# Performance work log

Measured on AMD Instinct MI355X. Metric: run time of the kernel, lower is better.

The kernel has to match this reference:

```python
import jax, jax.numpy as jnp
import numpy as np
from jax import lax

L, B, T_IMG, T_TXT = 12, 2, 256, 64
E, H, G = 1024, 16, 2730
V = 16416  # image_vocab_count + 1
C = E // H
EPS = 1e-6  # flax LayerNorm default


def _ln(x, scale, bias):
    mu = jnp.mean(x, -1, keepdims=True)
    var = jnp.var(x, -1, keepdims=True)
    y = (x - mu) * lax.rsqrt(var + EPS)
    if scale is not None:
        y = y * scale
    if bias is not None:
        y = y + bias
    return y


def _attend(k, v, q, mask, o_w):
    # k,v: [B,K,H,C]  q: [B,Q,H,C]  mask: [B,K]
    bias = jnp.where(mask, 0.0, -jnp.inf)[:, None, None, :]
    w = jnp.einsum('bqhc,bkhc->bhqk', q, k) + bias
    w = jax.nn.softmax(w, axis=-1)
    out = jnp.einsum('bhqk,bkhc->bqhc', w, v)
    return out.reshape(out.shape[0], out.shape[1], E) @ o_w


def setup_inputs():
    key = jax.random.key(0)
    ks = jax.random.split(key, 16)
    s = 0.02
    n = lambda k, shape: jax.random.normal(k, shape, jnp.float32) * s
    return dict(
        encoder_state=n(ks[0], (B, T_TXT, E)),
        keys_state=jnp.zeros((L, B, T_IMG, H, C), jnp.float32),
        values_state=jnp.zeros((L, B, T_IMG, H, C), jnp.float32),
        attention_mask=jnp.ones((B, T_TXT), jnp.bool_),
        prev_token=5000,
        token_index=100,
        embed_tok=n(ks[1], (V, E)),
        embed_pos=n(ks[2], (T_IMG, E)),
        ln_emb_s=jnp.ones((E,), jnp.float32),
        ln_emb_b=jnp.zeros((E,), jnp.float32),
        final_ln_b=jnp.zeros((E,), jnp.float32),
        lm_head_w=n(ks[3], (E, V)),
        pre_sa_ln_b=jnp.zeros((L, E), jnp.float32),
        sa_q_w=n(ks[4], (L, E, E)), sa_k_w=n(ks[5], (L, E, E)),
        sa_v_w=n(ks[6], (L, E, E)), sa_o_w=n(ks[7], (L, E, E)),
        sa_ln_s=jnp.ones((L, E), jnp.float32), sa_ln_b=jnp.zeros((L, E), jnp.float32),
        pre_ca_ln_b=jnp.zeros((L, E), jnp.float32),
        ca_q_w=n(ks[8], (L, E, E)), ca_k_w=n(ks[9], (L, E, E)),
        ca_v_w=n(ks[10], (L, E, E)), ca_o_w=n(ks[11], (L, E, E)),
        ca_ln_s=jnp.ones((L, E), jnp.float32), ca_ln_b=jnp.zeros((L, E), jnp.float32),
        glu_ln0_b=jnp.zeros((L, E), jnp.float32),
        glu_fc0_w=n(ks[12], (L, E, G)), glu_fc1_w=n(ks[13], (L, E, G)),
        glu_ln1_b=jnp.zeros((L, G), jnp.float32),
        glu_fc2_w=n(ks[14], (L, G, E)),
    )


def _decode_step(encoder_state, keys_state, values_state, attention_mask,
                 prev_token, token_index, embed_tok, embed_pos,
                 ln_emb_s, ln_emb_b, final_ln_b, lm_head_w, layer_params):
    ones = jnp.ones((B, 1), jnp.int32)
    ds = embed_tok[prev_token * ones] + embed_pos[token_index * ones]  # [B,1,E]
    ds = _ln(ds, ln_emb_s, ln_emb_b)
    self_mask = jnp.broadcast_to(jnp.arange(T_IMG) < token_index + 1, (B, T_IMG))
    scale = C ** 0.5

    def step(ds, xs):
        ks_l, vs_l, p = xs  # per-layer KV cache [B,T_IMG,H,C] and params
        (pre_sa_b, qw, kw, vw, ow, sa_s, sa_b,
         pre_ca_b, cqw, ckw, cvw, cow, ca_s, ca_b,
         g0b, f0, f1, g1b, f2) = p
        # --- self attention with KV-cache append ---
        residual = ds
        x = _ln(ds, None, pre_sa_b)
        ks_l = lax.dynamic_update_slice(ks_l, (x @ kw).reshape(B, 1, H, C), (0, token_index, 0, 0))
        vs_l = lax.dynamic_update_slice(vs_l, (x @ vw).reshape(B, 1, H, C), (0, token_index, 0, 0))
        q = (x @ qw).reshape(B, 1, H, C) / scale
        x = _attend(ks_l, vs_l, q, self_mask, ow)
        ds = residual + _ln(x, sa_s, sa_b)
        # --- cross attention over encoder state ---
        residual = ds
        x = _ln(ds, None, pre_ca_b)
        ek = (encoder_state @ ckw).reshape(B, T_TXT, H, C)
        ev = (encoder_state @ cvw).reshape(B, T_TXT, H, C)
        q = (x @ cqw).reshape(B, 1, H, C) / scale
        x = _attend(ek, ev, q, attention_mask, cow)
        ds = residual + _ln(x, ca_s, ca_b)
        # --- GLU FFN ---
        residual = ds
        z = _ln(ds, None, g0b)
        w = jax.nn.gelu(z @ f0, approximate=False)
        z = _ln(w * (z @ f1), None, g1b)
        ds = residual + z @ f2
        return ds, (ks_l, vs_l)

    ds, (keys_state, values_state) = lax.scan(step, ds, (keys_state, values_state, layer_params))
    ds = _ln(ds, None, final_ln_b)
    logits = ds @ lm_head_w  # [B,1,V]
    return logits, keys_state, values_state


def reference(encoder_state, keys_state, values_state, attention_mask, prev_token,
              token_index, embed_tok, embed_pos, ln_emb_s, ln_emb_b, final_ln_b,
              lm_head_w, pre_sa_ln_b, sa_q_w, sa_k_w, sa_v_w, sa_o_w, sa_ln_s,
              sa_ln_b, pre_ca_ln_b, ca_q_w, ca_k_w, ca_v_w, ca_o_w, ca_ln_s,
              ca_ln_b, glu_ln0_b, glu_fc0_w, glu_fc1_w, glu_ln1_b, glu_fc2_w):
    layer_params = (pre_sa_ln_b, sa_q_w, sa_k_w, sa_v_w, sa_o_w, sa_ln_s, sa_ln_b,
                    pre_ca_ln_b, ca_q_w, ca_k_w, ca_v_w, ca_o_w, ca_ln_s, ca_ln_b,
                    glu_ln0_b, glu_fc0_w, glu_fc1_w, glu_ln1_b, glu_fc2_w)
    return _decode_step(encoder_state, keys_state, values_state, attention_mask,
                        prev_token, token_index, embed_tok, embed_pos,
                        ln_emb_s, ln_emb_b, final_ln_b, lm_head_w, layer_params)
```

## Files before the change

### kernel.cpp

```cpp
#include <hip/hip_runtime.h>
#include <math.h>

#define LAYERS 12
#define EE 1024
#define GG 2730
#define VV 16416
#define EPS 1e-6f

#define OFF_DS 0
#define NSLOT 37
#define OFF_ACC (OFF_DS + NSLOT*2048)
#define ACC_STRIDE 28672
#define AQ 0
#define AK 2048
#define AV 4096
#define AY 6144
#define AQC 8192
#define ASC 10240
#define AOUT 12288
#define AY2 14336
#define AA 16384
#define AB2 21844
#define ACC_TOTAL (LAYERS*ACC_STRIDE)
#define ZERO_FLOATS (NSLOT*2048 + ACC_TOTAL)

#define KVL 524288
#define KVB 262144

struct MegaP {
  const float* enc; const float* keys_in; const float* values_in;
  const int* maski; const int* pt; const int* ti;
  const float* tok; const float* pos; const float* ln_s; const float* ln_b;
  const float* final_b; const float* lm_w;
  const float* pre_sa_b; const float* saq; const float* sak; const float* sav;
  const float* sao; const float* sas; const float* sab;
  const float* pre_ca_b; const float* caq; const float* ckw; const float* cvw;
  const float* cao; const float* cas; const float* cab;
  const float* g0b; const float* f0; const float* f1; const float* g1b; const float* f2;
  float* logits; float* keys_out; float* values_out; float* ws;
};

__device__ __forceinline__ void red4(float* sm, float& a, float& b, float& c, float& d){
  #pragma unroll
  for(int o=32;o;o>>=1){ a+=__shfl_down(a,o); b+=__shfl_down(b,o); c+=__shfl_down(c,o); d+=__shfl_down(d,o); }
  int w=threadIdx.x>>6, l=threadIdx.x&63;
  __syncthreads();
  if(l==0){ sm[w]=a; sm[4+w]=b; sm[8+w]=c; sm[12+w]=d; }
  __syncthreads();
  a=sm[0]+sm[1]+sm[2]+sm[3]; b=sm[4]+sm[5]+sm[6]+sm[7];
  c=sm[8]+sm[9]+sm[10]+sm[11]; d=sm[12]+sm[13]+sm[14]+sm[15];
}

__device__ __forceinline__ void ln_stats_g(const float* v, int K, float* sm,
    float& mu0, float& rs0, float& mu1, float& rs1){
  float s0=0,q0=0,s1=0,q1=0;
  for(int i=threadIdx.x;i<K;i+=256){ float a=v[i], b=v[K+i]; s0+=a;q0+=a*a;s1+=b;q1+=b*b; }
  red4(sm,s0,q0,s1,q1);
  mu0=s0/K; mu1=s1/K;
  rs0=rsqrtf(fmaxf(q0/K-mu0*mu0,0.f)+EPS);
  rs1=rsqrtf(fmaxf(q1/K-mu1*mu1,0.f)+EPS);
}

__device__ __forceinline__ void ln_stats_l(float (*Ds)[1024], float* sm,
    float& mu0, float& rs0, float& mu1, float& rs1){
  float s0=0,q0=0,s1=0,q1=0;
  for(int i=threadIdx.x;i<EE;i+=256){ float a=Ds[0][i], b=Ds[1][i]; s0+=a;q0+=a*a;s1+=b;q1+=b*b; }
  red4(sm,s0,q0,s1,q1);
  mu0=s0/EE; mu1=s1/EE;
  rs0=rsqrtf(fmaxf(q0/EE-mu0*mu0,0.f)+EPS);
  rs1=rsqrtf(fmaxf(q1/EE-mu1*mu1,0.f)+EPS);
}

__device__ __forceinline__ void build_ds3(const float* dsi, const float* accL,
    const float* sasl, const float* sabl, const float* casl, const float* cabl,
    float (*Ds)[1024], float* sm){
  float mu0,rs0,mu1,rs1;
  ln_stats_g(accL+AY, EE, sm, mu0,rs0,mu1,rs1);
  for(int i=threadIdx.x;i<EE;i+=256){ float sc=sasl[i], bi=sabl[i];
    Ds[0][i]=dsi[i]    + (accL[AY+i]-mu0)*rs0*sc + bi;
    Ds[1][i]=dsi[EE+i] + (accL[AY+EE+i]-mu1)*rs1*sc + bi; }
  ln_stats_g(accL+AY2, EE, sm, mu0,rs0,mu1,rs1);
  for(int i=threadIdx.x;i<EE;i+=256){ float sc=casl[i], bi=cabl[i];
    Ds[0][i] += (accL[AY2+i]-mu0)*rs0*sc + bi;
    Ds[1][i] += (accL[AY2+EE+i]-mu1)*rs1*sc + bi; }
}

__global__ __launch_bounds__(256)
void k_prelude(MegaP p){
  __shared__ float ev[EE];
  __shared__ float sm[16];
  const int t=threadIdx.x;
  int ptv = p.pt[0], tiv = p.ti[0];
  float s0=0,q0=0,d1=0,d2=0;
  for(int i=t;i<EE;i+=256){ float v=p.tok[(size_t)ptv*EE+i]+p.pos[(size_t)tiv*EE+i]; ev[i]=v; s0+=v; q0+=v*v; }
  red4(sm,s0,q0,d1,d2);
  float mu=s0/EE, rs=rsqrtf(fmaxf(q0/EE-mu*mu,0.f)+EPS);
  float* ds0 = p.ws + OFF_DS;
  __syncthreads();
  for(int i=t;i<EE;i+=256){ float y=(ev[i]-mu)*rs*p.ln_s[i]+p.ln_b[i]; ds0[i]=y; ds0[EE+i]=y; }
}

__global__ __launch_bounds__(256)
void k_qkv(MegaP p, int l){
  __shared__ float Xs[2][1024];
  __shared__ float sm[16];
  const int t=threadIdx.x, bx=blockIdx.x, by=blockIdx.y;
  if (bx >= 12){
    int cb = (bx-12)*64 + by;
    #pragma unroll
    for(int j=0;j<4;j++){
      int idx4 = cb*1024 + j*256 + t;
      int kv = idx4 >> 17;
      int r4 = idx4 & 131071;
      size_t off = (size_t)l*KVL + (size_t)r4*4;
      float4 v = *(const float4*)((kv? p.values_in : p.keys_in) + off);
      *(float4*)((kv? p.values_out : p.keys_out) + off) = v;
    }
    return;
  }
  const float* dsi = p.ws + OFF_DS + (size_t)(3*l)*2048;
  float* accL = p.ws + OFF_ACC + (size_t)l*ACC_STRIDE;
  const size_t lE2=(size_t)l*EE*EE, lE=(size_t)l*EE;
  int c = bx*256 + t;
  int sel = c>>10, cc = c&1023;
  const float* W = (sel==0? p.saq : sel==1? p.sak : p.sav) + lE2;
  float* O = accL + (sel==0? AQ : sel==1? AK : AV);
  int k0 = by*16;
  const float* wp = W + (size_t)k0*EE + cc;
  float wr[16];
  #pragma unroll
  for(int k=0;k<16;k++) wr[k] = wp[(size_t)k*EE];
  float mu0,rs0,mu1,rs1;
  ln_stats_g(dsi, EE, sm, mu0,rs0,mu1,rs1);
  for(int i=t;i<EE;i+=256){ float bi=p.pre_sa_b[lE+i];
    Xs[0][i]=(dsi[i]-mu0)*rs0+bi; Xs[1][i]=(dsi[EE+i]-mu1)*rs1+bi; }
  __syncthreads();
  float a0=0,a1=0;
  #pragma unroll
  for(int k=0;k<16;k++){ a0+=Xs[0][k0+k]*wr[k]; a1+=Xs[1][k0+k]*wr[k]; }
  atomicAdd(&O[cc],a0); atomicAdd(&O[EE+cc],a1);
}

__global__ __launch_bounds__(256)
void k_selfo(MegaP p, int l){
  __shared__ float Ds[2][1024];
  __shared__ float att[2][256];
  __shared__ float sm[16];
  const int t=threadIdx.x, bkid=blockIdx.x, tiv=p.ti[0];
  float* accL = p.ws + OFF_ACC + (size_t)l*ACC_STRIDE;
  const size_t lE2=(size_t)l*EE*EE;
  int cg=bkid&3, h=(bkid>>2)&15, sub=(bkid>>6)&3, hoff=h*64;
  if (t < 128){ int bb2=t>>6, c2=t&63; Ds[bb2][c2] = accL[AQ + bb2*EE + hoff + c2]*0.125f; }
  __syncthreads();
  for(int bb2=0;bb2<2;bb2++)
    for(int tt=t; tt<=tiv; tt+=256){
      const float* kr = (tt<tiv) ? (p.keys_in + (size_t)l*KVL + (size_t)bb2*KVB + (size_t)tt*EE + hoff)
                                 : (accL + AK + bb2*EE + hoff);
      float d=0;
      #pragma unroll
      for(int c2=0;c2<64;c2++) d += Ds[bb2][c2]*kr[c2];
      att[bb2][tt] = d;
    }
  __syncthreads();
  int wv=t>>6, l2=t&63;
  if (wv<2){
    float m=-3.4e38f;
    for(int tt=l2; tt<=tiv; tt+=64) m=fmaxf(m, att[wv][tt]);
    #pragma unroll
    for(int o=32;o;o>>=1) m=fmaxf(m,__shfl_xor(m,o));
    float s=0;
    for(int tt=l2; tt<=tiv; tt+=64){ float e=__expf(att[wv][tt]-m); att[wv][tt]=e; s+=e; }
    #pragma unroll
    for(int o=32;o;o>>=1) s+=__shfl_xor(s,o);
    if(l2==0) sm[8+wv]=1.f/s;
  }
  __syncthreads();
  {
    int bb2=t>>7, j=(t>>3)&15, part=t&7, colh=sub*16+j;
    float v=0;
    for(int tt=part; tt<=tiv; tt+=8){
      float vv = (tt<tiv)? p.values_in[(size_t)l*KVL + (size_t)bb2*KVB + (size_t)tt*EE + hoff + colh]
                         : accL[AV + bb2*EE + hoff + colh];
      v += att[bb2][tt]*vv;
    }
    v += __shfl_down(v,4,8); v += __shfl_down(v,2,8); v += __shfl_down(v,1,8);
    if(part==0) Ds[bb2][512+j] = v*sm[8+bb2];
  }
  __syncthreads();
  {
    int c = cg*256+t, kb = hoff + sub*16;
    const float* wp = p.sao + lE2 + (size_t)kb*EE + c;
    float a0=0,a1=0;
    #pragma unroll
    for(int j2=0;j2<16;j2++){ float w=wp[(size_t)j2*EE]; a0+=Ds[0][512+j2]*w; a1+=Ds[1][512+j2]*w; }
    atomicAdd(&accL[AY+c],a0); atomicAdd(&accL[AY+EE+c],a1);
  }
  if (cg==0 && sub==0){
    int bb2=t>>7, kv=(t>>6)&1, c2=t&63;
    float val = accL[(kv?AV:AK) + bb2*EE + hoff + c2];
    float* dst = (kv? p.values_out : p.keys_out)
               + (size_t)l*KVL + (size_t)bb2*KVB + (size_t)tiv*EE + hoff + c2;
    *dst = val;
  }
}

__global__ __launch_bounds__(256)
void k_ds2caq(MegaP p, int l){
  __shared__ float Xs[2][1024];
  __shared__ float Ds[2][1024];
  __shared__ float sm[16];
  const int t=threadIdx.x;
  const float* dsi = p.ws + OFF_DS + (size_t)(3*l)*2048;
  float* accL = p.ws + OFF_ACC + (size_t)l*ACC_STRIDE;
  const size_t lE2=(size_t)l*EE*EE, lE=(size_t)l*EE;
  int c = blockIdx.x*256 + t;
  int k0 = blockIdx.y*16;
  const float* wp = p.caq + lE2 + (size_t)k0*EE + c;
  float wr[16];
  #pragma unroll
  for(int k=0;k<16;k++) wr[k] = wp[(size_t)k*EE];
  float mu0,rs0,mu1,rs1;
  ln_stats_g(accL+AY, EE, sm, mu0,rs0,mu1,rs1);
  for(int i=t;i<EE;i+=256){ float sc=p.sas[lE+i], bi=p.sab[lE+i];
    Ds[0][i]=dsi[i]    + (accL[AY+i]-mu0)*rs0*sc + bi;
    Ds[1][i]=dsi[EE+i] + (accL[AY+EE+i]-mu1)*rs1*sc + bi; }
  ln_stats_l(Ds, sm, mu0,rs0,mu1,rs1);
  for(int i=t;i<EE;i+=256){ float bi=p.pre_ca_b[lE+i];
    Xs[0][i]=(Ds[0][i]-mu0)*rs0+bi; Xs[1][i]=(Ds[1][i]-mu1)*rs1+bi; }
  __syncthreads();
  float a0=0,a1=0;
  #pragma unroll
  for(int k=0;k<16;k++){ a0+=Xs[0][k0+k]*wr[k]; a1+=Xs[1][k0+k]*wr[k]; }
  float* O = accL + AQC;
  atomicAdd(&O[c],a0); atomicAdd(&O[EE+c],a1);
}

__global__ __launch_bounds__(256)
void k_uscore(MegaP p, int l){
  __shared__ float qs[64];
  __shared__ float us[256];
  const int t=threadIdx.x, bh=blockIdx.x, ec=blockIdx.y;
  const int b=bh>>4, h=bh&15, hoff=h*64;
  float* accL = p.ws + OFF_ACC + (size_t)l*ACC_STRIDE;
  const size_t lE2=(size_t)l*EE*EE;
  const int e = ec*256 + t;
  const float4* cp = (const float4*)(p.ckw + lE2 + (size_t)e*EE + hoff);
  float4 wr[16];
  #pragma unroll
  for(int j=0;j<16;j++) wr[j] = cp[j];
  if (t < 64) qs[t] = accL[AQC + b*EE + hoff + t]*0.125f;
  __syncthreads();
  float u=0;
  #pragma unroll
  for(int j=0;j<16;j++){
    u += wr[j].x*qs[4*j] + wr[j].y*qs[4*j+1] + wr[j].z*qs[4*j+2] + wr[j].w*qs[4*j+3];
  }
  us[t]=u;
  __syncthreads();
  int t2=t&63, q4=t>>6;
  const float4* ep = (const float4*)(p.enc + (size_t)(b*64+t2)*EE + ec*256 + q4*64);
  float pa=0;
  #pragma unroll
  for(int j=0;j<16;j++){
    float4 e4=ep[j];
    pa += e4.x*us[q4*64+4*j] + e4.y*us[q4*64+4*j+1] + e4.z*us[q4*64+4*j+2] + e4.w*us[q4*64+4*j+3];
  }
  atomicAdd(&accL[ASC + (b*16+h)*64 + t2], pa);
}

__global__ __launch_bounds__(256)
void k_ov(MegaP p, int l){
  __shared__ float att[64];
  __shared__ float ctxp[2][128];
  __shared__ float ctxs[128];
  __shared__ float smr[2];
  const int t=threadIdx.x, bh=blockIdx.x, es=blockIdx.y;
  const int b=bh>>4, h=bh&15, hoff=h*64, e0=es*128;
  float* accL = p.ws + OFF_ACC + (size_t)l*ACC_STRIDE;
  const size_t lE2=(size_t)l*EE*EE;
  const int c=t&63, part=t>>6;
  const float* vp = p.cvw + lE2 + (size_t)(e0+part*32)*EE + hoff + c;
  float wr[32];
  #pragma unroll
  for(int j=0;j<32;j++) wr[j] = vp[(size_t)j*EE];
  if (t<64){
    float sc = accL[ASC + (b*16+h)*64 + t];
    int mi=b*64+t;
    bool valid = (p.maski[mi]!=0) || (((const unsigned char*)p.maski)[mi]!=0);
    sc = valid? sc : -3.4e38f;
    float m=sc;
    #pragma unroll
    for(int o=32;o;o>>=1) m=fmaxf(m,__shfl_xor(m,o));
    float e_ = valid? __expf(sc-m) : 0.f;
    float s=e_;
    #pragma unroll
    for(int o=32;o;o>>=1) s+=__shfl_xor(s,o);
    att[t]=e_;
    if(t==0) smr[0]=1.f/s;
  }
  __syncthreads();
  {
    int e2=t>>1, half=t&1;
    const float* ep = p.enc + (size_t)(b*64+half*32)*EE + e0+e2;
    float ca=0;
    #pragma unroll 8
    for(int tt=0;tt<32;tt++) ca += att[half*32+tt]*ep[(size_t)tt*EE];
    ctxp[half][e2]=ca;
  }
  __syncthreads();
  if (t<128) ctxs[t] = (ctxp[0][t]+ctxp[1][t])*smr[0];
  __syncthreads();
  float a=0;
  #pragma unroll
  for(int j=0;j<32;j++) a += ctxs[part*32+j]*wr[j];
  atomicAdd(&accL[AOUT + b*EE + hoff + c], a);
}

__global__ __launch_bounds__(256)
void k_y2(MegaP p, int l){
  __shared__ float Xs[2][1024];
  const int t=threadIdx.x;
  float* accL = p.ws + OFF_ACC + (size_t)l*ACC_STRIDE;
  const size_t lE2=(size_t)l*EE*EE;
  int c = blockIdx.x*256 + t;
  int k0 = blockIdx.y*16;
  const float* wp = p.cao + lE2 + (size_t)k0*EE + c;
  float wr[16];
  #pragma unroll
  for(int k=0;k<16;k++) wr[k] = wp[(size_t)k*EE];
  for(int i=t;i<EE;i+=256){ Xs[0][i]=accL[AOUT+i]; Xs[1][i]=accL[AOUT+EE+i]; }
  __syncthreads();
  float a0=0,a1=0;
  #pragma unroll
  for(int k=0;k<16;k++){ a0+=Xs[0][k0+k]*wr[k]; a1+=Xs[1][k0+k]*wr[k]; }
  atomicAdd(&accL[AY2+c],a0); atomicAdd(&accL[AY2+EE+c],a1);
}

__global__ __launch_bounds__(256)
void k_glu01(MegaP p, int l){
  __shared__ float Xs[2][1024];
  __shared__ float Ds[2][1024];
  __shared__ float sm[16];
  const int t=threadIdx.x;
  const float* dsi = p.ws + OFF_DS + (size_t)(3*l)*2048;
  float* accL = p.ws + OFF_ACC + (size_t)l*ACC_STRIDE;
  const size_t lEG=(size_t)l*EE*GG, lE=(size_t)l*EE;
  int c2 = blockIdx.x*256 + t;
  int k0 = blockIdx.y*16;
  int sel=0, col=0;
  const float* W = nullptr;
  float2 wr[16];
  if (c2 < 2730){
    sel = (c2>=1365); int cc2 = sel? c2-1365 : c2; col = cc2*2;
    W = (sel? p.f1 : p.f0) + lEG;
    const float2* wp = (const float2*)(W + (size_t)k0*GG + col);
    #pragma unroll
    for(int k=0;k<16;k++) wr[k] = wp[(size_t)k*1365];
  }
  build_ds3(dsi, accL, p.sas+lE, p.sab+lE, p.cas+lE, p.cab+lE, Ds, sm);
  float mu0,rs0,mu1,rs1;
  ln_stats_l(Ds, sm, mu0,rs0,mu1,rs1);
  for(int i=t;i<EE;i+=256){ float bi=p.g0b[lE+i];
    Xs[0][i]=(Ds[0][i]-mu0)*rs0+bi; Xs[1][i]=(Ds[1][i]-mu1)*rs1+bi; }
  __syncthreads();
  if (c2 < 2730){
    float* O = accL + (sel? AB2 : AA);
    float a0=0,a1=0,b0=0,b1=0;
    #pragma unroll
    for(int k=0;k<16;k++){
      float x0=Xs[0][k0+k], x1=Xs[1][k0+k];
      a0+=x0*wr[k].x; a1+=x0*wr[k].y; b0+=x1*wr[k].x; b1+=x1*wr[k].y;
    }
    atomicAdd(&O[col+0],a0); atomicAdd(&O[col+1],a1);
    atomicAdd(&O[GG+col+0],b0); atomicAdd(&O[GG+col+1],b1);
  }
}

__global__ __launch_bounds__(256)
void k_glu2(MegaP p, int l){
  __shared__ float Xs[2][2736];
  __shared__ float Ds[2][1024];
  __shared__ float sm[16];
  const int t=threadIdx.x;
  const float* dsi = p.ws + OFF_DS + (size_t)(3*l)*2048;
  float* ds4 = p.ws + OFF_DS + (size_t)(3*l+3)*2048;
  float* accL = p.ws + OFF_ACC + (size_t)l*ACC_STRIDE;
  const size_t lGE=(size_t)l*GG*EE, lE=(size_t)l*EE, lG=(size_t)l*GG;
  const int ks = blockIdx.y;
  int c = blockIdx.x*256 + t;
  int k0 = ks*32, k1 = k0+32; if (k1>GG) k1=GG;
  const float* wp = p.f2 + lGE + (size_t)k0*EE + c;
  float wr[32];
  #pragma unroll
  for(int k=0;k<32;k++) wr[k] = (k0+k<GG) ? wp[(size_t)k*EE] : 0.f;
  if (ks==0) build_ds3(dsi, accL, p.sas+lE, p.sab+lE, p.cas+lE, p.cab+lE, Ds, sm);
  float s0=0,q0=0,s1=0,q1=0;
  for(int i=t;i<GG;i+=256){
    float a0v=accL[AA+i], a1v=accL[AA+GG+i];
    float b0v=accL[AB2+i], b1v=accL[AB2+GG+i];
    float g0v=0.5f*a0v*(1.f+erff(a0v*0.70710678118654752f));
    float g1v=0.5f*a1v*(1.f+erff(a1v*0.70710678118654752f));
    float t0=g0v*b0v, t1=g1v*b1v;
    Xs[0][i]=t0; Xs[1][i]=t1;
    s0+=t0;q0+=t0*t0;s1+=t1;q1+=t1*t1;
  }
  red4(sm,s0,q0,s1,q1);
  float mu0=s0/GG, mu1=s1/GG;
  float rs0=rsqrtf(fmaxf(q0/GG-mu0*mu0,0.f)+EPS), rs1=rsqrtf(fmaxf(q1/GG-mu1*mu1,0.f)+EPS);
  for(int i=t;i<GG;i+=256){ float bi=p.g1b[lG+i];
    Xs[0][i]=(Xs[0][i]-mu0)*rs0+bi; Xs[1][i]=(Xs[1][i]-mu1)*rs1+bi; }
  __syncthreads();
  float a0=0,b0=0;
  if (ks==0){ a0=Ds[0][c]; b0=Ds[1][c]; }
  #pragma unroll
  for(int k=0;k<32;k++){
    if (k0+k<GG){ a0+=Xs[0][k0+k]*wr[k]; b0+=Xs[1][k0+k]*wr[k]; }
  }
  atomicAdd(&ds4[c],a0); atomicAdd(&ds4[EE+c],b0);
}

__global__ __launch_bounds__(256)
void k_lm(MegaP p){
  __shared__ float Xs[2][1024];
  __shared__ float sm[16];
  const int t=threadIdx.x;
  const float* dsf = p.ws + OFF_DS + (size_t)36*2048;
  float mu0,rs0,mu1,rs1;
  ln_stats_g(dsf, EE, sm, mu0,rs0,mu1,rs1);
  for(int i=t;i<EE;i+=256){ float bi=p.final_b[i];
    Xs[0][i]=(dsf[i]-mu0)*rs0+bi; Xs[1][i]=(dsf[EE+i]-mu1)*rs1+bi; }
  __syncthreads();
  int c4 = blockIdx.x*256 + t;
  if (c4 < 4104){
    int col = c4*4;
    int k0 = blockIdx.y*32;
    const float4* wp = (const float4*)(p.lm_w + (size_t)k0*VV + col);
    float a0=0,a1=0,a2=0,a3=0,b0=0,b1=0,b2=0,b3=0;
    #pragma unroll 8
    for(int k=0;k<32;k++){
      float4 w=*wp; wp+=4104;
      float x0=Xs[0][k0+k], x1=Xs[1][k0+k];
      a0+=x0*w.x; a1+=x0*w.y; a2+=x0*w.z; a3+=x0*w.w;
      b0+=x1*w.x; b1+=x1*w.y; b2+=x1*w.z; b3+=x1*w.w;
    }
    atomicAdd(&p.logits[col+0],a0); atomicAdd(&p.logits[col+1],a1);
    atomicAdd(&p.logits[col+2],a2); atomicAdd(&p.logits[col+3],a3);
    atomicAdd(&p.logits[VV+col+0],b0); atomicAdd(&p.logits[VV+col+1],b1);
    atomicAdd(&p.logits[VV+col+2],b2); atomicAdd(&p.logits[VV+col+3],b3);
  }
}

extern "C" void kernel_launch(void* const* d_in, const int* in_sizes, int n_in,
                              void* d_out, int out_size, void* d_ws, size_t ws_size,
                              hipStream_t stream){
  (void)in_sizes; (void)n_in; (void)out_size; (void)ws_size;
  float* out = (float*)d_out;
  float* ws = (float*)d_ws;

  MegaP P;
  P.enc        = (const float*)d_in[0];
  P.keys_in    = (const float*)d_in[1];
  P.values_in  = (const float*)d_in[2];
  P.maski      = (const int*)d_in[3];
  P.pt         = (const int*)d_in[4];
  P.ti         = (const int*)d_in[5];
  P.tok        = (const float*)d_in[6];
  P.pos        = (const float*)d_in[7];
  P.ln_s       = (const float*)d_in[8];
  P.ln_b       = (const float*)d_in[9];
  P.final_b    = (const float*)d_in[10];
  P.lm_w       = (const float*)d_in[11];
  P.pre_sa_b   = (const float*)d_in[12];
  P.saq        = (const float*)d_in[13];
  P.sak        = (const float*)d_in[14];
  P.sav        = (const float*)d_in[15];
  P.sao        = (const float*)d_in[16];
  P.sas        = (const float*)d_in[17];
  P.sab        = (const float*)d_in[18];
  P.pre_ca_b   = (const float*)d_in[19];
  P.caq        = (const float*)d_in[20];
  P.ckw        = (const float*)d_in[21];
  P.cvw        = (const float*)d_in[22];
  P.cao        = (const float*)d_in[23];
  P.cas        = (const float*)d_in[24];
  P.cab        = (const float*)d_in[25];
  P.g0b        = (const float*)d_in[26];
  P.f0         = (const float*)d_in[27];
  P.f1         = (const float*)d_in[28];
  P.g1b        = (const float*)d_in[29];
  P.f2         = (const float*)d_in[30];
  P.logits     = out;
  P.keys_out   = out + (size_t)2*VV;
  P.values_out = P.keys_out + (size_t)LAYERS*KVL;
  P.ws         = ws;

  hipMemsetAsync(ws + OFF_DS, 0, (size_t)ZERO_FLOATS*sizeof(float), stream);
  hipMemsetAsync(P.logits, 0, (size_t)2*VV*sizeof(float), stream);

  k_prelude<<<1,256,0,stream>>>(P);
  for (int l=0;l<LAYERS;l++){
    k_qkv   <<<dim3(16,64),256,0,stream>>>(P,l);
    k_selfo <<<256,        256,0,stream>>>(P,l);
    k_ds2caq<<<dim3(4,64), 256,0,stream>>>(P,l);
    k_uscore<<<dim3(32,4), 256,0,stream>>>(P,l);
    k_ov    <<<dim3(32,8), 256,0,stream>>>(P,l);
    k_y2    <<<dim3(4,64), 256,0,stream>>>(P,l);
    k_glu01 <<<dim3(11,64),256,0,stream>>>(P,l);
    k_glu2  <<<dim3(4,86), 256,0,stream>>>(P,l);
  }
  k_lm<<<dim3(17,32),256,0,stream>>>(P);
}
```

Baseline: 1.065 ms.

## Fuse cross-attention chain into one per-head kernel with 1024 threads

Replaces the four cross-attention kernels (LN plus Q projection, key-score, softmax plus value/output, output projection) with one kernel. Each of the 32 blocks handles one (batch, head) pair and keeps all intermediates in shared memory. This removes three launches and the global atomic round trips between stages per layer. In exchange only 32 blocks run, each streaming its own head slice of four weight matrices through serialized phases, with Q and K weights read once per batch. That risks low GPU occupancy and a latency-bound weight stream.

```diff
diff --git a/kernel.cpp b/kernel.cpp
--- a/kernel.cpp
+++ b/kernel.cpp
@@ -51,6 +51,18 @@
   c=sm[8]+sm[9]+sm[10]+sm[11]; d=sm[12]+sm[13]+sm[14]+sm[15];
 }
 
+__device__ __forceinline__ void red2_1024(float* sm, float& a, float& b){
+  #pragma unroll
+  for(int o=32;o;o>>=1){ a+=__shfl_down(a,o); b+=__shfl_down(b,o); }
+  int w=threadIdx.x>>6, l=threadIdx.x&63;
+  __syncthreads();
+  if(l==0){ sm[w]=a; sm[16+w]=b; }
+  __syncthreads();
+  a=0; b=0;
+  #pragma unroll
+  for(int j=0;j<16;j++){ a+=sm[j]; b+=sm[16+j]; }
+}
+
 __device__ __forceinline__ void ln_stats_g(const float* v, int K, float* sm,
     float& mu0, float& rs0, float& mu1, float& rs1){
   float s0=0,q0=0,s1=0,q1=0;
@@ -204,136 +216,124 @@
   }
 }
 
-__global__ __launch_bounds__(256)
-void k_ds2caq(MegaP p, int l){
-  __shared__ float Xs[2][1024];
-  __shared__ float Ds[2][1024];
-  __shared__ float sm[16];
-  const int t=threadIdx.x;
+__global__ __launch_bounds__(1024)
+void k_cross(MegaP p, int l){
+  __shared__ float Xs[1024];
+  __shared__ float P[1024];
+  __shared__ float us[1024];
+  __shared__ float Cx[1024];
+  __shared__ float att[64];
+  __shared__ float outh[64];
+  __shared__ float sm[32];
+  const int t=threadIdx.x, bi=blockIdx.x;
+  const int b=bi>>4, h=bi&15, hoff=h*64;
+  float* accL = p.ws + OFF_ACC + (size_t)l*ACC_STRIDE;
   const float* dsi = p.ws + OFF_DS + (size_t)(3*l)*2048;
-  float* accL = p.ws + OFF_ACC + (size_t)l*ACC_STRIDE;
   const size_t lE2=(size_t)l*EE*EE, lE=(size_t)l*EE;
-  int c = blockIdx.x*256 + t;
-  int k0 = blockIdx.y*16;
-  const float* wp = p.caq + lE2 + (size_t)k0*EE + c;
-  float wr[16];
-  #pragma unroll
-  for(int k=0;k<16;k++) wr[k] = wp[(size_t)k*EE];
-  float mu0,rs0,mu1,rs1;
-  ln_stats_g(accL+AY, EE, sm, mu0,rs0,mu1,rs1);
-  for(int i=t;i<EE;i+=256){ float sc=p.sas[lE+i], bi=p.sab[lE+i];
-    Ds[0][i]=dsi[i]    + (accL[AY+i]-mu0)*rs0*sc + bi;
-    Ds[1][i]=dsi[EE+i] + (accL[AY+EE+i]-mu1)*rs1*sc + bi; }
-  ln_stats_l(Ds, sm, mu0,rs0,mu1,rs1);
-  for(int i=t;i<EE;i+=256){ float bi=p.pre_ca_b[lE+i];
-    Xs[0][i]=(Ds[0][i]-mu0)*rs0+bi; Xs[1][i]=(Ds[1][i]-mu1)*rs1+bi; }
-  __syncthreads();
-  float a0=0,a1=0;
-  #pragma unroll
-  for(int k=0;k<16;k++){ a0+=Xs[0][k0+k]*wr[k]; a1+=Xs[1][k0+k]*wr[k]; }
-  float* O = accL + AQC;
-  atomicAdd(&O[c],a0); atomicAdd(&O[EE+c],a1);
-}
-
-__global__ __launch_bounds__(256)
-void k_uscore(MegaP p, int l){
-  __shared__ float qs[64];
-  __shared__ float us[256];
-  const int t=threadIdx.x, bh=blockIdx.x, ec=blockIdx.y;
-  const int b=bh>>4, h=bh&15, hoff=h*64;
-  float* accL = p.ws + OFF_ACC + (size_t)l*ACC_STRIDE;
-  const size_t lE2=(size_t)l*EE*EE;
-  const int e = ec*256 + t;
-  const float4* cp = (const float4*)(p.ckw + lE2 + (size_t)e*EE + hoff);
-  float4 wr[16];
-  #pragma unroll
-  for(int j=0;j<16;j++) wr[j] = cp[j];
-  if (t < 64) qs[t] = accL[AQC + b*EE + hoff + t]*0.125f;
-  __syncthreads();
-  float u=0;
-  #pragma unroll
-  for(int j=0;j<16;j++){
-    u += wr[j].x*qs[4*j] + wr[j].y*qs[4*j+1] + wr[j].z*qs[4*j+2] + wr[j].w*qs[4*j+3];
-  }
-  us[t]=u;
-  __syncthreads();
-  int t2=t&63, q4=t>>6;
-  const float4* ep = (const float4*)(p.enc + (size_t)(b*64+t2)*EE + ec*256 + q4*64);
-  float pa=0;
-  #pragma unroll
-  for(int j=0;j<16;j++){
-    float4 e4=ep[j];
-    pa += e4.x*us[q4*64+4*j] + e4.y*us[q4*64+4*j+1] + e4.z*us[q4*64+4*j+2] + e4.w*us[q4*64+4*j+3];
-  }
-  atomicAdd(&accL[ASC + (b*16+h)*64 + t2], pa);
-}
-
-__global__ __launch_bounds__(256)
-void k_ov(MegaP p, int l){
-  __shared__ float att[64];
-  __shared__ float ctxp[2][128];
-  __shared__ float ctxs[128];
-  __shared__ float smr[2];
-  const int t=threadIdx.x, bh=blockIdx.x, es=blockIdx.y;
-  const int b=bh>>4, h=bh&15, hoff=h*64, e0=es*128;
-  float* accL = p.ws + OFF_ACC + (size_t)l*ACC_STRIDE;
-  const size_t lE2=(size_t)l*EE*EE;
-  const int c=t&63, part=t>>6;
-  const float* vp = p.cvw + lE2 + (size_t)(e0+part*32)*EE + hoff + c;
-  float wr[32];
-  #pragma unroll
-  for(int j=0;j<32;j++) wr[j] = vp[(size_t)j*EE];
+
+  float yv = accL[AY + b*EE + t];
+  float s0=yv, q0=yv*yv;
+  red2_1024(sm, s0, q0);
+  float mu=s0/EE, rs=rsqrtf(fmaxf(q0/EE-mu*mu,0.f)+EPS);
+  float ds2v = dsi[b*EE+t] + (yv-mu)*rs*p.sas[lE+t] + p.sab[lE+t];
+  s0=ds2v; q0=ds2v*ds2v;
+  __syncthreads();
+  red2_1024(sm, s0, q0);
+  mu=s0/EE; rs=rsqrtf(fmaxf(q0/EE-mu*mu,0.f)+EPS);
+  Xs[t] = (ds2v-mu)*rs + p.pre_ca_b[lE+t];
+  __syncthreads();
+
+  {
+    int c=t&63, kp=t>>6;
+    const float* cqp = p.caq + lE2 + (size_t)(kp*64)*EE + hoff + c;
+    float pq=0;
+    #pragma unroll 8
+    for(int j=0;j<64;j++) pq += Xs[kp*64+j]*cqp[(size_t)j*EE];
+    P[t]=pq;
+  }
+  __syncthreads();
   if (t<64){
-    float sc = accL[ASC + (b*16+h)*64 + t];
+    float q=0;
+    #pragma unroll
+    for(int kp=0;kp<16;kp++) q += P[kp*64+t];
+    us[t] = q*0.125f;
+  }
+  __syncthreads();
+  if (t<64) att[t]=us[t];
+  __syncthreads();
+
+  {
+    const float4* ckp = (const float4*)(p.ckw + lE2 + (size_t)t*EE + hoff);
+    float u=0;
+    #pragma unroll
+    for(int j=0;j<16;j++){
+      float4 w=ckp[j];
+      u += w.x*att[4*j] + w.y*att[4*j+1] + w.z*att[4*j+2] + w.w*att[4*j+3];
+    }
+    us[t]=u;
+  }
+  __syncthreads();
+
+  {
+    int tt=t>>4, ep=t&15;
+    const float* erow = p.enc + (size_t)(b*64+tt)*EE + ep*64;
+    float ps=0;
+    #pragma unroll 8
+    for(int j=0;j<64;j++) ps += us[ep*64+j]*erow[j];
+    P[t]=ps;
+  }
+  __syncthreads();
+  if (t<64){
+    float sc=0;
+    #pragma unroll
+    for(int ep=0;ep<16;ep++) sc += P[t*16+ep];
     int mi=b*64+t;
     bool valid = (p.maski[mi]!=0) || (((const unsigned char*)p.maski)[mi]!=0);
     sc = valid? sc : -3.4e38f;
     float m=sc;
     #pragma unroll
     for(int o=32;o;o>>=1) m=fmaxf(m,__shfl_xor(m,o));
-    float e_ = valid? __expf(sc-m) : 0.f;
+    float e_=valid? __expf(sc-m):0.f;
     float s=e_;
     #pragma unroll
     for(int o=32;o;o>>=1) s+=__shfl_xor(s,o);
-    att[t]=e_;
-    if(t==0) smr[0]=1.f/s;
-  }
-  __syncthreads();
-  {
-    int e2=t>>1, half=t&1;
-    const float* ep = p.enc + (size_t)(b*64+half*32)*EE + e0+e2;
-    float ca=0;
+    att[t]=e_/s;
+  }
+  __syncthreads();
+
+  {
+    const float* encB = p.enc + (size_t)(b*64)*EE + t;
+    float cv=0;
     #pragma unroll 8
-    for(int tt=0;tt<32;tt++) ca += att[half*32+tt]*ep[(size_t)tt*EE];
-    ctxp[half][e2]=ca;
-  }
-  __syncthreads();
-  if (t<128) ctxs[t] = (ctxp[0][t]+ctxp[1][t])*smr[0];
-  __syncthreads();
-  float a=0;
-  #pragma unroll
-  for(int j=0;j<32;j++) a += ctxs[part*32+j]*wr[j];
-  atomicAdd(&accL[AOUT + b*EE + hoff + c], a);
-}
-
-__global__ __launch_bounds__(256)
-void k_y2(MegaP p, int l){
-  __shared__ float Xs[2][1024];
-  const int t=threadIdx.x;
-  float* accL = p.ws + OFF_ACC + (size_t)l*ACC_STRIDE;
-  const size_t lE2=(size_t)l*EE*EE;
-  int c = blockIdx.x*256 + t;
-  int k0 = blockIdx.y*16;
-  const float* wp = p.cao + lE2 + (size_t)k0*EE + c;
-  float wr[16];
-  #pragma unroll
-  for(int k=0;k<16;k++) wr[k] = wp[(size_t)k*EE];
-  for(int i=t;i<EE;i+=256){ Xs[0][i]=accL[AOUT+i]; Xs[1][i]=accL[AOUT+EE+i]; }
-  __syncthreads();
-  float a0=0,a1=0;
-  #pragma unroll
-  for(int k=0;k<16;k++){ a0+=Xs[0][k0+k]*wr[k]; a1+=Xs[1][k0+k]*wr[k]; }
-  atomicAdd(&accL[AY2+c],a0); atomicAdd(&accL[AY2+EE+c],a1);
+    for(int tt=0;tt<64;tt++) cv += att[tt]*encB[(size_t)tt*EE];
+    Cx[t]=cv;
+  }
+  __syncthreads();
+
+  {
+    int c=t&63, ep=t>>6;
+    const float* cvp = p.cvw + lE2 + (size_t)(ep*64)*EE + hoff + c;
+    float po=0;
+    #pragma unroll 8
+    for(int j=0;j<64;j++) po += Cx[ep*64+j]*cvp[(size_t)j*EE];
+    P[t]=po;
+  }
+  __syncthreads();
+  if (t<64){
+    float o=0;
+    #pragma unroll
+    for(int ep=0;ep<16;ep++) o += P[ep*64+t];
+    outh[t]=o;
+  }
+  __syncthreads();
+
+  {
+    const float* cop = p.cao + lE2 + (size_t)hoff*EE + t;
+    float y=0;
+    #pragma unroll 8
+    for(int c2=0;c2<64;c2++) y += outh[c2]*cop[(size_t)c2*EE];
+    atomicAdd(&accL[AY2 + b*EE + t], y);
+  }
 }
 
 __global__ __launch_bounds__(256)
@@ -501,10 +501,7 @@
   for (int l=0;l<LAYERS;l++){
     k_qkv   <<<dim3(16,64),256,0,stream>>>(P,l);
     k_selfo <<<256,        256,0,stream>>>(P,l);
-    k_ds2caq<<<dim3(4,64), 256,0,stream>>>(P,l);
-    k_uscore<<<dim3(32,4), 256,0,stream>>>(P,l);
-    k_ov    <<<dim3(32,8), 256,0,stream>>>(P,l);
-    k_y2    <<<dim3(4,64), 256,0,stream>>>(P,l);
+    k_cross <<<32,        1024,0,stream>>>(P,l);
     k_glu01 <<<dim3(11,64),256,0,stream>>>(P,l);
     k_glu2  <<<dim3(4,86), 256,0,stream>>>(P,l);
   }
```

After: 1.271 ms. 1.19x slower.

## Fuse cross-attn value and output projections; vectorize weight loads in GEMV kernels

Applied to the files above, without the earlier changes.

Merges the cross-attention context/value kernel and the output-projection kernel into one. Each block now projects its partial per-head output straight through its 64-row slice of the output weights and atomically accumulates into the residual, which removes one launch and the AOUT round trip. The QKV, cross-attention query and GLU fc2 GEMVs switch to float4/float2 weight loads with several columns per thread, and their grids and K-splits are re-shaped to match; the KV cache copy moves into one column of QKV blocks. The cost is that the fused kernel re-reads each head's output-weight slice from every (batch, e-slice) block and issues many more atomics.

```diff
diff --git a/kernel.cpp b/kernel.cpp
--- a/kernel.cpp
+++ b/kernel.cpp
@@ -17,7 +17,6 @@
 #define AY 6144
 #define AQC 8192
 #define ASC 10240
-#define AOUT 12288
 #define AY2 14336
 #define AA 16384
 #define AB2 21844
@@ -105,11 +104,11 @@
   __shared__ float Xs[2][1024];
   __shared__ float sm[16];
   const int t=threadIdx.x, bx=blockIdx.x, by=blockIdx.y;
-  if (bx >= 12){
-    int cb = (bx-12)*64 + by;
-    #pragma unroll
-    for(int j=0;j<4;j++){
-      int idx4 = cb*1024 + j*256 + t;
+  if (bx == 3){
+    int cb = by;
+    #pragma unroll
+    for(int j=0;j<8;j++){
+      int idx4 = cb*2048 + j*256 + t;
       int kv = idx4 >> 17;
       int r4 = idx4 & 131071;
       size_t off = (size_t)l*KVL + (size_t)r4*4;
@@ -121,24 +120,29 @@
   const float* dsi = p.ws + OFF_DS + (size_t)(3*l)*2048;
   float* accL = p.ws + OFF_ACC + (size_t)l*ACC_STRIDE;
   const size_t lE2=(size_t)l*EE*EE, lE=(size_t)l*EE;
-  int c = bx*256 + t;
-  int sel = c>>10, cc = c&1023;
+  int c4 = bx*256 + t;
+  int col = c4*4, sel = col>>10, cc = col&1023;
   const float* W = (sel==0? p.saq : sel==1? p.sak : p.sav) + lE2;
   float* O = accL + (sel==0? AQ : sel==1? AK : AV);
-  int k0 = by*16;
-  const float* wp = W + (size_t)k0*EE + cc;
-  float wr[16];
-  #pragma unroll
-  for(int k=0;k<16;k++) wr[k] = wp[(size_t)k*EE];
+  int k0 = by*8;
+  const float4* wp = (const float4*)(W + (size_t)k0*EE + cc);
+  float4 wr[8];
+  #pragma unroll
+  for(int k=0;k<8;k++) wr[k] = wp[(size_t)k*256];
   float mu0,rs0,mu1,rs1;
   ln_stats_g(dsi, EE, sm, mu0,rs0,mu1,rs1);
   for(int i=t;i<EE;i+=256){ float bi=p.pre_sa_b[lE+i];
     Xs[0][i]=(dsi[i]-mu0)*rs0+bi; Xs[1][i]=(dsi[EE+i]-mu1)*rs1+bi; }
   __syncthreads();
-  float a0=0,a1=0;
-  #pragma unroll
-  for(int k=0;k<16;k++){ a0+=Xs[0][k0+k]*wr[k]; a1+=Xs[1][k0+k]*wr[k]; }
-  atomicAdd(&O[cc],a0); atomicAdd(&O[EE+cc],a1);
+  float a0=0,a1=0,a2=0,a3=0,b0=0,b1=0,b2=0,b3=0;
+  #pragma unroll
+  for(int k=0;k<8;k++){
+    float x0=Xs[0][k0+k], x1=Xs[1][k0+k];
+    a0+=x0*wr[k].x; a1+=x0*wr[k].y; a2+=x0*wr[k].z; a3+=x0*wr[k].w;
+    b0+=x1*wr[k].x; b1+=x1*wr[k].y; b2+=x1*wr[k].z; b3+=x1*wr[k].w;
+  }
+  atomicAdd(&O[cc+0],a0); atomicAdd(&O[cc+1],a1); atomicAdd(&O[cc+2],a2); atomicAdd(&O[cc+3],a3);
+  atomicAdd(&O[EE+cc+0],b0); atomicAdd(&O[EE+cc+1],b1); atomicAdd(&O[EE+cc+2],b2); atomicAdd(&O[EE+cc+3],b3);
 }
 
 __global__ __launch_bounds__(256)
@@ -213,12 +217,12 @@
   const float* dsi = p.ws + OFF_DS + (size_t)(3*l)*2048;
   float* accL = p.ws + OFF_ACC + (size_t)l*ACC_STRIDE;
   const size_t lE2=(size_t)l*EE*EE, lE=(size_t)l*EE;
-  int c = blockIdx.x*256 + t;
-  int k0 = blockIdx.y*16;
-  const float* wp = p.caq + lE2 + (size_t)k0*EE + c;
-  float wr[16];
-  #pragma unroll
-  for(int k=0;k<16;k++) wr[k] = wp[(size_t)k*EE];
+  int col = t*4;
+  int k0 = blockIdx.x*4;
+  const float4* wp = (const float4*)(p.caq + lE2 + (size_t)k0*EE + col);
+  float4 wr[4];
+  #pragma unroll
+  for(int k=0;k<4;k++) wr[k] = wp[(size_t)k*256];
   float mu0,rs0,mu1,rs1;
   ln_stats_g(accL+AY, EE, sm, mu0,rs0,mu1,rs1);
   for(int i=t;i<EE;i+=256){ float sc=p.sas[lE+i], bi=p.sab[lE+i];
@@ -228,11 +232,16 @@
   for(int i=t;i<EE;i+=256){ float bi=p.pre_ca_b[lE+i];
     Xs[0][i]=(Ds[0][i]-mu0)*rs0+bi; Xs[1][i]=(Ds[1][i]-mu1)*rs1+bi; }
   __syncthreads();
-  float a0=0,a1=0;
-  #pragma unroll
-  for(int k=0;k<16;k++){ a0+=Xs[0][k0+k]*wr[k]; a1+=Xs[1][k0+k]*wr[k]; }
+  float a0=0,a1=0,a2=0,a3=0,b0=0,b1=0,b2=0,b3=0;
+  #pragma unroll
+  for(int k=0;k<4;k++){
+    float x0=Xs[0][k0+k], x1=Xs[1][k0+k];
+    a0+=x0*wr[k].x; a1+=x0*wr[k].y; a2+=x0*wr[k].z; a3+=x0*wr[k].w;
+    b0+=x1*wr[k].x; b1+=x1*wr[k].y; b2+=x1*wr[k].z; b3+=x1*wr[k].w;
+  }
   float* O = accL + AQC;
-  atomicAdd(&O[c],a0); atomicAdd(&O[EE+c],a1);
+  atomicAdd(&O[col+0],a0); atomicAdd(&O[col+1],a1); atomicAdd(&O[col+2],a2); atomicAdd(&O[col+3],a3);
+  atomicAdd(&O[EE+col+0],b0); atomicAdd(&O[EE+col+1],b1); atomicAdd(&O[EE+col+2],b2); atomicAdd(&O[EE+col+3],b3);
 }
 
 __global__ __launch_bounds__(256)
@@ -269,11 +278,12 @@
 }
 
 __global__ __launch_bounds__(256)
-void k_ov(MegaP p, int l){
+void k_ovy2(MegaP p, int l){
   __shared__ float att[64];
   __shared__ float ctxp[2][128];
   __shared__ float ctxs[128];
-  __shared__ float smr[2];
+  __shared__ float P[256];
+  __shared__ float outh[64];
   const int t=threadIdx.x, bh=blockIdx.x, es=blockIdx.y;
   const int b=bh>>4, h=bh&15, hoff=h*64, e0=es*128;
   float* accL = p.ws + OFF_ACC + (size_t)l*ACC_STRIDE;
@@ -295,8 +305,7 @@
     float s=e_;
     #pragma unroll
     for(int o=32;o;o>>=1) s+=__shfl_xor(s,o);
-    att[t]=e_;
-    if(t==0) smr[0]=1.f/s;
+    att[t]=e_/s;
   }
   __syncthreads();
   {
@@ -308,32 +317,26 @@
     ctxp[half][e2]=ca;
   }
   __syncthreads();
-  if (t<128) ctxs[t] = (ctxp[0][t]+ctxp[1][t])*smr[0];
-  __syncthreads();
-  float a=0;
-  #pragma unroll
-  for(int j=0;j<32;j++) a += ctxs[part*32+j]*wr[j];
-  atomicAdd(&accL[AOUT + b*EE + hoff + c], a);
-}
-
-__global__ __launch_bounds__(256)
-void k_y2(MegaP p, int l){
-  __shared__ float Xs[2][1024];
-  const int t=threadIdx.x;
-  float* accL = p.ws + OFF_ACC + (size_t)l*ACC_STRIDE;
-  const size_t lE2=(size_t)l*EE*EE;
-  int c = blockIdx.x*256 + t;
-  int k0 = blockIdx.y*16;
-  const float* wp = p.cao + lE2 + (size_t)k0*EE + c;
-  float wr[16];
-  #pragma unroll
-  for(int k=0;k<16;k++) wr[k] = wp[(size_t)k*EE];
-  for(int i=t;i<EE;i+=256){ Xs[0][i]=accL[AOUT+i]; Xs[1][i]=accL[AOUT+EE+i]; }
-  __syncthreads();
-  float a0=0,a1=0;
-  #pragma unroll
-  for(int k=0;k<16;k++){ a0+=Xs[0][k0+k]*wr[k]; a1+=Xs[1][k0+k]*wr[k]; }
-  atomicAdd(&accL[AY2+c],a0); atomicAdd(&accL[AY2+EE+c],a1);
+  if (t<128) ctxs[t] = ctxp[0][t]+ctxp[1][t];
+  __syncthreads();
+  {
+    float po=0;
+    #pragma unroll
+    for(int j=0;j<32;j++) po += ctxs[part*32+j]*wr[j];
+    P[t]=po;
+  }
+  __syncthreads();
+  if (t<64) outh[t] = P[t]+P[64+t]+P[128+t]+P[192+t];
+  __syncthreads();
+  {
+    const float* cop = p.cao + lE2 + (size_t)hoff*EE;
+    for(int n=t;n<EE;n+=256){
+      float y=0;
+      #pragma unroll 8
+      for(int c2=0;c2<64;c2++) y += outh[c2]*cop[(size_t)c2*EE + n];
+      atomicAdd(&accL[AY2 + b*EE + n], y);
+    }
+  }
 }
 
 __global__ __launch_bounds__(256)
@@ -387,12 +390,16 @@
   float* accL = p.ws + OFF_ACC + (size_t)l*ACC_STRIDE;
   const size_t lGE=(size_t)l*GG*EE, lE=(size_t)l*EE, lG=(size_t)l*GG;
   const int ks = blockIdx.y;
-  int c = blockIdx.x*256 + t;
-  int k0 = ks*32, k1 = k0+32; if (k1>GG) k1=GG;
-  const float* wp = p.f2 + lGE + (size_t)k0*EE + c;
-  float wr[32];
-  #pragma unroll
-  for(int k=0;k<32;k++) wr[k] = (k0+k<GG) ? wp[(size_t)k*EE] : 0.f;
+  int c2 = blockIdx.x*256 + t;
+  int col = c2*2;
+  int k0 = ks*16;
+  const float2* wp = (const float2*)(p.f2 + lGE + (size_t)k0*EE + col);
+  float2 wr[16];
+  #pragma unroll
+  for(int k=0;k<16;k++){
+    if (k0+k < GG) wr[k] = wp[(size_t)k*512];
+    else { wr[k].x=0.f; wr[k].y=0.f; }
+  }
   if (ks==0) build_ds3(dsi, accL, p.sas+lE, p.sab+lE, p.cas+lE, p.cab+lE, Ds, sm);
   float s0=0,q0=0,s1=0,q1=0;
   for(int i=t;i<GG;i+=256){
@@ -410,13 +417,17 @@
   for(int i=t;i<GG;i+=256){ float bi=p.g1b[lG+i];
     Xs[0][i]=(Xs[0][i]-mu0)*rs0+bi; Xs[1][i]=(Xs[1][i]-mu1)*rs1+bi; }
   __syncthreads();
-  float a0=0,b0=0;
-  if (ks==0){ a0=Ds[0][c]; b0=Ds[1][c]; }
-  #pragma unroll
-  for(int k=0;k<32;k++){
-    if (k0+k<GG){ a0+=Xs[0][k0+k]*wr[k]; b0+=Xs[1][k0+k]*wr[k]; }
-  }
-  atomicAdd(&ds4[c],a0); atomicAdd(&ds4[EE+c],b0);
+  float a0=0,a1=0,b0=0,b1=0;
+  if (ks==0){ a0=Ds[0][col]; a1=Ds[0][col+1]; b0=Ds[1][col]; b1=Ds[1][col+1]; }
+  #pragma unroll
+  for(int k=0;k<16;k++){
+    if (k0+k < GG){
+      float x0=Xs[0][k0+k], x1=Xs[1][k0+k];
+      a0+=x0*wr[k].x; a1+=x0*wr[k].y; b0+=x1*wr[k].x; b1+=x1*wr[k].y;
+    }
+  }
+  atomicAdd(&ds4[col+0],a0); atomicAdd(&ds4[col+1],a1);
+  atomicAdd(&ds4[EE+col+0],b0); atomicAdd(&ds4[EE+col+1],b1);
 }
 
 __global__ __launch_bounds__(256)
@@ -499,14 +510,13 @@
 
   k_prelude<<<1,256,0,stream>>>(P);
   for (int l=0;l<LAYERS;l++){
-    k_qkv   <<<dim3(16,64),256,0,stream>>>(P,l);
+    k_qkv   <<<dim3(4,128),256,0,stream>>>(P,l);
     k_selfo <<<256,        256,0,stream>>>(P,l);
-    k_ds2caq<<<dim3(4,64), 256,0,stream>>>(P,l);
+    k_ds2caq<<<256,        256,0,stream>>>(P,l);
     k_uscore<<<dim3(32,4), 256,0,stream>>>(P,l);
-    k_ov    <<<dim3(32,8), 256,0,stream>>>(P,l);
-    k_y2    <<<dim3(4,64), 256,0,stream>>>(P,l);
+    k_ovy2  <<<dim3(32,8), 256,0,stream>>>(P,l);
     k_glu01 <<<dim3(11,64),256,0,stream>>>(P,l);
-    k_glu2  <<<dim3(4,86), 256,0,stream>>>(P,l);
+    k_glu2  <<<dim3(2,171),256,0,stream>>>(P,l);
   }
   k_lm<<<dim3(17,32),256,0,stream>>>(P);
 }
```

After: 1.910 ms. 1.79x slower.

## Fuse cross-attention query projection into per-head score kernel

Applied to the files above, without the earlier changes.

Merges the LN + cross-attention Q projection kernel into the score kernel: each (batch, head, e-chunk) block recomputes the two layernorms for its batch row and computes its head's 64 query columns directly, removing one launch per layer and the atomic accumulation into a global Q buffer. The exchange is redundant work: each Q head slice (1024x64 weights) is now read by 4 blocks instead of once, and the layernorm is recomputed by all 128 blocks. It targets launch and serialization overhead in a latency-bound decode step.

```diff
diff --git a/kernel.cpp b/kernel.cpp
--- a/kernel.cpp
+++ b/kernel.cpp
@@ -15,7 +15,6 @@
 #define AK 2048
 #define AV 4096
 #define AY 6144
-#define AQC 8192
 #define ASC 10240
 #define AOUT 12288
 #define AY2 14336
@@ -205,58 +204,76 @@
 }
 
 __global__ __launch_bounds__(256)
-void k_ds2caq(MegaP p, int l){
-  __shared__ float Xs[2][1024];
-  __shared__ float Ds[2][1024];
-  __shared__ float sm[16];
-  const int t=threadIdx.x;
-  const float* dsi = p.ws + OFF_DS + (size_t)(3*l)*2048;
-  float* accL = p.ws + OFF_ACC + (size_t)l*ACC_STRIDE;
-  const size_t lE2=(size_t)l*EE*EE, lE=(size_t)l*EE;
-  int c = blockIdx.x*256 + t;
-  int k0 = blockIdx.y*16;
-  const float* wp = p.caq + lE2 + (size_t)k0*EE + c;
-  float wr[16];
-  #pragma unroll
-  for(int k=0;k<16;k++) wr[k] = wp[(size_t)k*EE];
-  float mu0,rs0,mu1,rs1;
-  ln_stats_g(accL+AY, EE, sm, mu0,rs0,mu1,rs1);
-  for(int i=t;i<EE;i+=256){ float sc=p.sas[lE+i], bi=p.sab[lE+i];
-    Ds[0][i]=dsi[i]    + (accL[AY+i]-mu0)*rs0*sc + bi;
-    Ds[1][i]=dsi[EE+i] + (accL[AY+EE+i]-mu1)*rs1*sc + bi; }
-  ln_stats_l(Ds, sm, mu0,rs0,mu1,rs1);
-  for(int i=t;i<EE;i+=256){ float bi=p.pre_ca_b[lE+i];
-    Xs[0][i]=(Ds[0][i]-mu0)*rs0+bi; Xs[1][i]=(Ds[1][i]-mu1)*rs1+bi; }
-  __syncthreads();
-  float a0=0,a1=0;
-  #pragma unroll
-  for(int k=0;k<16;k++){ a0+=Xs[0][k0+k]*wr[k]; a1+=Xs[1][k0+k]*wr[k]; }
-  float* O = accL + AQC;
-  atomicAdd(&O[c],a0); atomicAdd(&O[EE+c],a1);
-}
-
-__global__ __launch_bounds__(256)
-void k_uscore(MegaP p, int l){
+void k_qscore(MegaP p, int l){
+  __shared__ float Xs[1024];
+  __shared__ float P[16][64];
   __shared__ float qs[64];
   __shared__ float us[256];
+  __shared__ float sm[16];
   const int t=threadIdx.x, bh=blockIdx.x, ec=blockIdx.y;
   const int b=bh>>4, h=bh&15, hoff=h*64;
   float* accL = p.ws + OFF_ACC + (size_t)l*ACC_STRIDE;
-  const size_t lE2=(size_t)l*EE*EE;
-  const int e = ec*256 + t;
-  const float4* cp = (const float4*)(p.ckw + lE2 + (size_t)e*EE + hoff);
-  float4 wr[16];
-  #pragma unroll
-  for(int j=0;j<16;j++) wr[j] = cp[j];
-  if (t < 64) qs[t] = accL[AQC + b*EE + hoff + t]*0.125f;
-  __syncthreads();
-  float u=0;
-  #pragma unroll
-  for(int j=0;j<16;j++){
-    u += wr[j].x*qs[4*j] + wr[j].y*qs[4*j+1] + wr[j].z*qs[4*j+2] + wr[j].w*qs[4*j+3];
-  }
-  us[t]=u;
-  __syncthreads();
+  const float* dsi = p.ws + OFF_DS + (size_t)(3*l)*2048;
+  const size_t lE2=(size_t)l*EE*EE, lE=(size_t)l*EE;
+  const int w=t>>6, ln=t&63;
+
+  float s0=0,q0=0;
+  for(int i=t;i<EE;i+=256){ float v=accL[AY+b*EE+i]; s0+=v; q0+=v*v; }
+  #pragma unroll
+  for(int o=32;o;o>>=1){ s0+=__shfl_down(s0,o); q0+=__shfl_down(q0,o); }
+  if(ln==0){ sm[w]=s0; sm[4+w]=q0; }
+  __syncthreads();
+  float mu=(sm[0]+sm[1]+sm[2]+sm[3])/EE;
+  float qq=(sm[4]+sm[5]+sm[6]+sm[7])/EE;
+  float rs=rsqrtf(fmaxf(qq-mu*mu,0.f)+EPS);
+  float s1=0,q1=0;
+  for(int i=t;i<EE;i+=256){
+    float d = dsi[b*EE+i] + (accL[AY+b*EE+i]-mu)*rs*p.sas[lE+i] + p.sab[lE+i];
+    Xs[i]=d; s1+=d; q1+=d*d;
+  }
+  #pragma unroll
+  for(int o=32;o;o>>=1){ s1+=__shfl_down(s1,o); q1+=__shfl_down(q1,o); }
+  if(ln==0){ sm[8+w]=s1; sm[12+w]=q1; }
+  __syncthreads();
+  float mu2=(sm[8]+sm[9]+sm[10]+sm[11])/EE;
+  float q2=(sm[12]+sm[13]+sm[14]+sm[15])/EE;
+  float rs2=rsqrtf(fmaxf(q2-mu2*mu2,0.f)+EPS);
+  for(int i=t;i<EE;i+=256) Xs[i] = (Xs[i]-mu2)*rs2 + p.pre_ca_b[lE+i];
+  __syncthreads();
+
+  {
+    int c4=t&15, kr=t>>4;
+    const float4* cq = (const float4*)(p.caq + lE2 + (size_t)kr*EE + hoff) + c4;
+    float ax=0,ay=0,az=0,aw=0;
+    #pragma unroll 8
+    for(int i=0;i<64;i++){
+      float4 wv = cq[(size_t)i*16*256];
+      float x = Xs[kr+16*i];
+      ax+=x*wv.x; ay+=x*wv.y; az+=x*wv.z; aw+=x*wv.w;
+    }
+    P[kr][c4*4+0]=ax; P[kr][c4*4+1]=ay; P[kr][c4*4+2]=az; P[kr][c4*4+3]=aw;
+  }
+  __syncthreads();
+  if (t<64){
+    float qv=0;
+    #pragma unroll
+    for(int kr=0;kr<16;kr++) qv += P[kr][t];
+    qs[t] = qv*0.125f;
+  }
+  __syncthreads();
+
+  {
+    const float4* ckp = (const float4*)(p.ckw + lE2 + (size_t)(ec*256+t)*EE + hoff);
+    float u=0;
+    #pragma unroll
+    for(int j=0;j<16;j++){
+      float4 wv=ckp[j];
+      u += wv.x*qs[4*j] + wv.y*qs[4*j+1] + wv.z*qs[4*j+2] + wv.w*qs[4*j+3];
+    }
+    us[t]=u;
+  }
+  __syncthreads();
+
   int t2=t&63, q4=t>>6;
   const float4* ep = (const float4*)(p.enc + (size_t)(b*64+t2)*EE + ec*256 + q4*64);
   float pa=0;
@@ -501,8 +518,7 @@
   for (int l=0;l<LAYERS;l++){
     k_qkv   <<<dim3(16,64),256,0,stream>>>(P,l);
     k_selfo <<<256,        256,0,stream>>>(P,l);
-    k_ds2caq<<<dim3(4,64), 256,0,stream>>>(P,l);
-    k_uscore<<<dim3(32,4), 256,0,stream>>>(P,l);
+    k_qscore<<<dim3(32,4), 256,0,stream>>>(P,l);
     k_ov    <<<dim3(32,8), 256,0,stream>>>(P,l);
     k_y2    <<<dim3(4,64), 256,0,stream>>>(P,l);
     k_glu01 <<<dim3(11,64),256,0,stream>>>(P,l);
```

Measured after the change: 1.075 ms. About the same (+0.9%).
